# Performance work log

Hardware: AMD Instinct MI355X
Metric: run time of the kernel (lower is better)

The kernel has to match this reference:

```python
import jax, jax.numpy as jnp
import numpy as np

CHUNK = 64  # mamba chunk size


def _ssd_chunk_scan(x, dt, A, Bs, Cs, R):
    """Exact chunked selective scan (mamba_chunk_scan_combined math, no D skip).
    x: [B,L,H,P] (H=K*R heads), dt: [B,L,H] (already softplus'd),
    A: [H], Bs/Cs: [B,L,K,N] groups (head h uses group h//R).
    Returns y: [B,L,H,P]."""
    Bsz, L, Hh, P = x.shape
    K, N = Bs.shape[2], Bs.shape[3]
    Nc = L // CHUNK
    # broadcast groups -> heads (head k*R+r uses group k)
    Bh = jnp.repeat(Bs, R, axis=2)  # [B,L,H,N]
    Ch = jnp.repeat(Cs, R, axis=2)
    xc = x.reshape(Bsz, Nc, CHUNK, Hh, P)
    dtc = dt.reshape(Bsz, Nc, CHUNK, Hh)
    Bc = Bh.reshape(Bsz, Nc, CHUNK, Hh, N)
    Cc = Ch.reshape(Bsz, Nc, CHUNK, Hh, N)
    dA = jnp.transpose(dtc, (0, 1, 3, 2)) * A[None, None, :, None]  # [B,Nc,H,Q]
    Acum = jnp.cumsum(dA, axis=-1)
    # intra-chunk decay matrix Lmat[i,j] = exp(sum_{j<s<=i} dA_s), lower-tri
    diff = Acum[..., :, None] - Acum[..., None, :]  # [B,Nc,H,Q,Q]
    tri = jnp.tril(jnp.ones((CHUNK, CHUNK), bool))
    Lmat = jnp.where(tri, jnp.exp(diff), 0.0)
    xdt = xc * dtc[..., None]  # dt enters as dt_j * B_j * x_j
    Y_diag = jnp.einsum('bcqhn,bcshn,bchqs,bcshp->bcqhp', Cc, Bc, Lmat, xdt)
    # chunk end states
    decay_last = jnp.exp(Acum[..., -1:] - Acum)  # [B,Nc,H,Q]
    states = jnp.einsum('bcqhn,bchq,bcqhp->bchpn', Bc, decay_last, xdt)
    chunk_decay = jnp.exp(Acum[..., -1])  # [B,Nc,H]
    def step(S, inp):
        cd, st = inp
        return cd[..., None, None] * S + st, S  # emit state BEFORE this chunk
    S0 = jnp.zeros((Bsz, Hh, P, N), x.dtype)
    _, prev = jax.lax.scan(step, S0, (jnp.moveaxis(chunk_decay, 1, 0), jnp.moveaxis(states, 1, 0)))
    prev = jnp.moveaxis(prev, 0, 1)  # [B,Nc,H,P,N]
    Y_off = jnp.einsum('bcqhn,bchpn,bchq->bcqhp', Cc, prev, jnp.exp(Acum))
    return (Y_diag + Y_off).reshape(Bsz, L, Hh, P)


def _forward(x, in_proj_w, conv_w, conv_b, x_proj_w, A_logs, Ds, dt_bias,
             out_norm_g, out_norm_b, out_proj_w):
    B, H, W, Dm = x.shape
    K, R = A_logs.shape
    P = Ds.shape[2]               # headdim
    d_inner = x_proj_w.shape[2]
    N = (x_proj_w.shape[1] - R) // 2
    L = H * W
    # in_proj + gate split
    xz = jnp.einsum('bhwc,dc->bhwd', x, in_proj_w)
    xi, z = jnp.split(xz, 2, axis=-1)
    z = jax.nn.gelu(z, approximate=False)
    # depthwise 3x3 conv (torch weight [d_inner,1,3,3] -> HWIO [3,3,1,d_inner])
    kern = jnp.transpose(conv_w, (2, 3, 1, 0))
    xi = jax.lax.conv_general_dilated(xi, kern, (1, 1), 'SAME',
            dimension_numbers=('NHWC', 'HWIO', 'NHWC'),
            feature_group_count=d_inner) + conv_b
    xi = jax.nn.gelu(xi, approximate=False)
    # cross2d scan: row-major, col-major, and their reverses
    x0 = xi.reshape(B, L, d_inner)
    x1 = jnp.transpose(xi, (0, 2, 1, 3)).reshape(B, L, d_inner)
    xs = jnp.stack([x0, x1, x0[:, ::-1], x1[:, ::-1]], axis=2)  # [B,L,K,d_inner]
    x_dbl = jnp.einsum('blkd,kcd->blkc', xs, x_proj_w)
    dts = x_dbl[..., :R].reshape(B, L, K * R)
    Bs = x_dbl[..., R:R + N]
    Cs = x_dbl[..., R + N:]
    xs_h = xs.reshape(B, L, K * R, P)
    A = -jnp.exp(A_logs.astype(jnp.float32)).reshape(K * R)
    Dmat = Ds.astype(jnp.float32).reshape(K * R, P)
    dt = jax.nn.softplus(dts + dt_bias.reshape(K * R))
    ys = _ssd_chunk_scan(xs_h, dt, A, Bs, Cs, R) + xs_h * Dmat  # D skip on raw x
    ys = ys.reshape(B, L, K, d_inner)
    # cross merge: invert each scan order, sum over K
    def unT(y):
        return jnp.transpose(y.reshape(B, W, H, d_inner), (0, 2, 1, 3)).reshape(B, L, d_inner)
    y = ys[:, :, 0] + ys[:, ::-1, 2] + unT(ys[:, :, 1]) + unT(ys[:, ::-1, 3])
    # out LayerNorm
    y = y.reshape(B, H, W, d_inner)
    mu = y.mean(-1, keepdims=True)
    var = y.var(-1, keepdims=True)
    y = (y - mu) / jnp.sqrt(var + 1e-5) * out_norm_g + out_norm_b
    y = y * z  # gating
    return jnp.einsum('bhwd,cd->bhwc', y, out_proj_w)


def setup_inputs() -> dict:
    key = jax.random.key(0)
    ks = jax.random.split(key, 10)
    B, H, W, Dm = 2, 64, 64, 192
    d_inner, K, R, N = 384, 4, 12, 64
    P = d_inner // R  # 32
    s = 0.02
    return {
        'x': jax.random.normal(ks[0], (B, H, W, Dm), jnp.float32),
        'in_proj_w': s * jax.random.normal(ks[1], (2 * d_inner, Dm), jnp.float32),
        'conv_w': s * jax.random.normal(ks[2], (d_inner, 1, 3, 3), jnp.float32),
        'conv_b': s * jax.random.normal(ks[3], (d_inner,), jnp.float32),
        'x_proj_w': s * jax.random.normal(ks[4], (K, R + 2 * N, d_inner), jnp.float32),
        'A_logs': 0.5 * jax.random.normal(ks[5], (K, R), jnp.float32),
        'Ds': jax.random.uniform(ks[6], (K, R, P), jnp.float32),
        'dt_bias': 0.1 * jax.random.uniform(ks[7], (K, R), jnp.float32),
        'out_norm_g': jnp.ones((d_inner,), jnp.float32),
        'out_norm_b': jnp.zeros((d_inner,), jnp.float32),
        'out_proj_w': s * jax.random.normal(ks[8], (Dm, d_inner), jnp.float32),
    }


def reference(x, in_proj_w, conv_w, conv_b, x_proj_w, A_logs, Ds, dt_bias,
              out_norm_g, out_norm_b, out_proj_w):
    return _forward(x, in_proj_w, conv_w, conv_b, x_proj_w, A_logs, Ds, dt_bias,
                    out_norm_g, out_norm_b, out_proj_w)
```

## Files before the change

### kernel.cpp

```cpp
#include <hip/hip_runtime.h>
#include <math.h>

#define DI 384

typedef __attribute__((ext_vector_type(8))) short bf8v;
typedef __attribute__((ext_vector_type(4))) float f4v;

__device__ __forceinline__ f4v mfma16(bf8v a, bf8v b, f4v c) {
  return __builtin_amdgcn_mfma_f32_16x16x32_bf16(a, b, c, 0, 0, 0);
}

__device__ __forceinline__ int trf(int l) { return ((l & 63) << 6) | (l >> 6); }
__device__ __forceinline__ int mapk(int k, int l) {
  if (k == 0) return l;
  if (k == 1) return trf(l);
  if (k == 2) return 4095 - l;
  return trf(4095 - l);
}
__device__ __forceinline__ float gelu_f(float x) {
  return 0.5f * x * (1.0f + erff(x * 0.7071067811865475f));
}
__device__ __forceinline__ float softplus_f(float x) {
  return (x > 20.0f) ? x : log1pf(expf(x));
}
__device__ __forceinline__ unsigned short f2bf(float f) {
  unsigned u = __float_as_uint(f);
  unsigned r = (u + 0x7fff + ((u >> 16) & 1)) >> 16;
  return (unsigned short)r;
}
__device__ __forceinline__ float bf2f(unsigned short h) {
  return __uint_as_float(((unsigned)h) << 16);
}
__device__ __forceinline__ int swz(int row, int col) {
  return (row << 6) + ((((col >> 3) ^ (row & 7)) << 3) | (col & 7));
}
__device__ __forceinline__ int foff(int row, int cb) {
  return (row << 6) + ((cb ^ (row & 7)) << 3);
}

__global__ __launch_bounds__(256) void k_cvt(const float* __restrict__ src,
                                             unsigned short* __restrict__ hi,
                                             unsigned short* __restrict__ lo, int n) {
  int i = blockIdx.x * 256 + threadIdx.x;
  if (i >= n) return;
  float v = src[i];
  unsigned short h = f2bf(v);
  hi[i] = h;
  lo[i] = f2bf(v - bf2f(h));
}

__global__ __launch_bounds__(256) void k_inproj(const unsigned short* __restrict__ Ahi,
                                                const unsigned short* __restrict__ Alo,
                                                const unsigned short* __restrict__ Whi,
                                                const unsigned short* __restrict__ Wlo,
                                                float* __restrict__ xi_raw,
                                                float* __restrict__ zg) {
  const int K = 192;
  __shared__ unsigned short Ah[4096], Al[4096], Bh[4096], Bl[4096];
  int tid = threadIdx.x;
  int lane = tid & 63, w = tid >> 6;
  int cl = lane & 15, kb = lane >> 4;
  int wm = w >> 1, wn = w & 1;
  int m0 = blockIdx.y * 64, n0 = blockIdx.x * 64;
  f4v acc[2][2];
  acc[0][0] = acc[0][1] = acc[1][0] = acc[1][1] = (f4v){0.f, 0.f, 0.f, 0.f};
  for (int k0 = 0; k0 < K; k0 += 64) {
#pragma unroll
    for (int u = 0; u < 2; ++u) {
      int unit = tid + u * 256;
      int row = unit >> 3, blk = unit & 7;
      int e = foff(row, blk);
      size_t ga = (size_t)(m0 + row) * K + k0 + blk * 8;
      size_t gb = (size_t)(n0 + row) * K + k0 + blk * 8;
      *(bf8v*)(Ah + e) = *(const bf8v*)(Ahi + ga);
      *(bf8v*)(Al + e) = *(const bf8v*)(Alo + ga);
      *(bf8v*)(Bh + e) = *(const bf8v*)(Whi + gb);
      *(bf8v*)(Bl + e) = *(const bf8v*)(Wlo + gb);
    }
    __syncthreads();
#pragma unroll
    for (int chunk = 0; chunk < 2; ++chunk) {
      int cb = chunk * 4 + kb;
      bf8v ah[2], al[2], bh[2], bl[2];
#pragma unroll
      for (int mi = 0; mi < 2; ++mi) {
        ah[mi] = *(const bf8v*)(Ah + foff(wm * 32 + mi * 16 + cl, cb));
        al[mi] = *(const bf8v*)(Al + foff(wm * 32 + mi * 16 + cl, cb));
      }
#pragma unroll
      for (int ni = 0; ni < 2; ++ni) {
        bh[ni] = *(const bf8v*)(Bh + foff(wn * 32 + ni * 16 + cl, cb));
        bl[ni] = *(const bf8v*)(Bl + foff(wn * 32 + ni * 16 + cl, cb));
      }
#pragma unroll
      for (int mi = 0; mi < 2; ++mi)
#pragma unroll
        for (int ni = 0; ni < 2; ++ni) {
          acc[mi][ni] = mfma16(ah[mi], bh[ni], acc[mi][ni]);
          acc[mi][ni] = mfma16(ah[mi], bl[ni], acc[mi][ni]);
          acc[mi][ni] = mfma16(al[mi], bh[ni], acc[mi][ni]);
        }
    }
    __syncthreads();
  }
#pragma unroll
  for (int mi = 0; mi < 2; ++mi)
#pragma unroll
    for (int ni = 0; ni < 2; ++ni)
#pragma unroll
      for (int i = 0; i < 4; ++i) {
        int m = m0 + wm * 32 + mi * 16 + kb * 4 + i;
        int n = n0 + wn * 32 + ni * 16 + cl;
        float v = acc[mi][ni][i];
        if (n < DI) xi_raw[(size_t)m * DI + n] = v;
        else zg[(size_t)m * DI + (n - DI)] = gelu_f(v);
      }
}

__global__ __launch_bounds__(256) void k_conv(const float* __restrict__ xin,
                                              const float* __restrict__ cw,
                                              const float* __restrict__ cb,
                                              unsigned short* __restrict__ xhi,
                                              unsigned short* __restrict__ xlo) {
  int idx = blockIdx.x * 256 + threadIdx.x;
  int c = idx % DI;
  int lf = idx / DI;
  int b = lf >> 12;
  int l = lf & 4095;
  int h = l >> 6, w = l & 63;
  float acc = cb[c];
#pragma unroll
  for (int dh = -1; dh <= 1; ++dh) {
    int hh = h + dh;
    if ((unsigned)hh >= 64u) continue;
#pragma unroll
    for (int dw = -1; dw <= 1; ++dw) {
      int ww = w + dw;
      if ((unsigned)ww >= 64u) continue;
      acc += xin[((size_t)((b << 12) | (hh << 6) | ww)) * DI + c] *
             cw[c * 9 + (dh + 1) * 3 + (dw + 1)];
    }
  }
  float g = gelu_f(acc);
  unsigned short hv = f2bf(g);
  xhi[(size_t)idx] = hv;
  xlo[(size_t)idx] = f2bf(g - bf2f(hv));
}

__global__ __launch_bounds__(256) void k_xproj(const unsigned short* __restrict__ xhi,
                                               const unsigned short* __restrict__ xlo,
                                               const unsigned short* __restrict__ Whi,
                                               const unsigned short* __restrict__ Wlo,
                                               const float* __restrict__ dt_bias,
                                               float* __restrict__ dt_buf,
                                               unsigned short* __restrict__ Bhi,
                                               unsigned short* __restrict__ Blo,
                                               unsigned short* __restrict__ Chi,
                                               unsigned short* __restrict__ Clo) {
  const int K = DI, N = 140;
  int kdir = blockIdx.z;
  __shared__ unsigned short Ah[4096], Al[4096], Bh[4096], Bl[4096];
  __shared__ int rowbase[64];
  int tid = threadIdx.x;
  int lane = tid & 63, w = tid >> 6;
  int cl = lane & 15, kb = lane >> 4;
  int wm = w >> 1, wn = w & 1;
  int m0 = blockIdx.y * 64, n0 = blockIdx.x * 64;
  if (tid < 64) {
    int m = m0 + tid;
    int b = m >> 12, l = m & 4095;
    rowbase[tid] = (b << 12) + mapk(kdir, l);
  }
  const unsigned short* wkh = Whi + (size_t)kdir * N * K;
  const unsigned short* wkl = Wlo + (size_t)kdir * N * K;
  f4v acc[2][2];
  acc[0][0] = acc[0][1] = acc[1][0] = acc[1][1] = (f4v){0.f, 0.f, 0.f, 0.f};
  __syncthreads();
  for (int k0 = 0; k0 < K; k0 += 64) {
#pragma unroll
    for (int u = 0; u < 2; ++u) {
      int unit = tid + u * 256;
      int row = unit >> 3, blk = unit & 7;
      int e = foff(row, blk);
      size_t ga = (size_t)rowbase[row] * K + k0 + blk * 8;
      *(bf8v*)(Ah + e) = *(const bf8v*)(xhi + ga);
      *(bf8v*)(Al + e) = *(const bf8v*)(xlo + ga);
      int n = n0 + row;
      if (n < N) {
        size_t gb = (size_t)n * K + k0 + blk * 8;
        *(bf8v*)(Bh + e) = *(const bf8v*)(wkh + gb);
        *(bf8v*)(Bl + e) = *(const bf8v*)(wkl + gb);
      } else {
        bf8v z = {0, 0, 0, 0, 0, 0, 0, 0};
        *(bf8v*)(Bh + e) = z;
        *(bf8v*)(Bl + e) = z;
      }
    }
    __syncthreads();
#pragma unroll
    for (int chunk = 0; chunk < 2; ++chunk) {
      int cb = chunk * 4 + kb;
      bf8v ah[2], al[2], bh[2], bl[2];
#pragma unroll
      for (int mi = 0; mi < 2; ++mi) {
        ah[mi] = *(const bf8v*)(Ah + foff(wm * 32 + mi * 16 + cl, cb));
        al[mi] = *(const bf8v*)(Al + foff(wm * 32 + mi * 16 + cl, cb));
      }
#pragma unroll
      for (int ni = 0; ni < 2; ++ni) {
        bh[ni] = *(const bf8v*)(Bh + foff(wn * 32 + ni * 16 + cl, cb));
        bl[ni] = *(const bf8v*)(Bl + foff(wn * 32 + ni * 16 + cl, cb));
      }
#pragma unroll
      for (int mi = 0; mi < 2; ++mi)
#pragma unroll
        for (int ni = 0; ni < 2; ++ni) {
          acc[mi][ni] = mfma16(ah[mi], bh[ni], acc[mi][ni]);
          acc[mi][ni] = mfma16(ah[mi], bl[ni], acc[mi][ni]);
          acc[mi][ni] = mfma16(al[mi], bh[ni], acc[mi][ni]);
        }
    }
    __syncthreads();
  }
#pragma unroll
  for (int mi = 0; mi < 2; ++mi)
#pragma unroll
    for (int ni = 0; ni < 2; ++ni)
#pragma unroll
      for (int i = 0; i < 4; ++i) {
        int m = m0 + wm * 32 + mi * 16 + kb * 4 + i;
        int n = n0 + wn * 32 + ni * 16 + cl;
        if (n >= N) continue;
        float v = acc[mi][ni][i];
        int b = m >> 12, l = m & 4095;
        if (n < 12) {
          dt_buf[(((size_t)(b * 48 + kdir * 12 + n)) << 12) + l] =
              softplus_f(v + dt_bias[kdir * 12 + n]);
        } else if (n < 76) {
          size_t off = (((size_t)((b * 4 + kdir) << 12)) + l) * 64 + (n - 12);
          unsigned short hh = f2bf(v);
          Bhi[off] = hh;
          Blo[off] = f2bf(v - bf2f(hh));
        } else {
          size_t off = (((size_t)((b * 4 + kdir) << 12)) + l) * 64 + (n - 76);
          unsigned short hh = f2bf(v);
          Chi[off] = hh;
          Clo[off] = f2bf(v - bf2f(hh));
        }
      }
}

__global__ __launch_bounds__(256) void k_states(const unsigned short* __restrict__ xhi,
                                                const unsigned short* __restrict__ xlo,
                                                const float* __restrict__ dt_buf,
                                                const unsigned short* __restrict__ Bhi,
                                                const unsigned short* __restrict__ Blo,
                                                const float* __restrict__ A_logs,
                                                unsigned short* __restrict__ Shi,
                                                float* __restrict__ cdec) {
  int c = blockIdx.x, k = blockIdx.y >> 1, g = blockIdx.y & 1, b = blockIdx.z;
  __shared__ unsigned short Bt_h[4096], Bt_l[4096];
  __shared__ unsigned short xw_h[2048], xw_l[2048];
  int tid = threadIdx.x;
  int lane = tid & 63, w = tid >> 6;
  int cl = lane & 15, kb = lane >> 4;
  size_t Bbase = (((size_t)((b * 4 + k) << 12)) + c * 64) * 64;
  {
    int n = lane;
#pragma unroll
    for (int it = 0; it < 8; ++it) {
      int q0 = 2 * (w + it * 4);
      unsigned short h0 = Bhi[Bbase + (size_t)q0 * 64 + n];
      unsigned short h1 = Bhi[Bbase + (size_t)(q0 + 1) * 64 + n];
      unsigned short l0 = Blo[Bbase + (size_t)q0 * 64 + n];
      unsigned short l1 = Blo[Bbase + (size_t)(q0 + 1) * 64 + n];
      int e = swz(n, q0);
      *(unsigned int*)(Bt_h + e) = (unsigned)h0 | ((unsigned)h1 << 16);
      *(unsigned int*)(Bt_l + e) = (unsigned)l0 | ((unsigned)l1 << 16);
    }
  }
  int p_s = tid & 31, qg = tid >> 5;
  for (int rr = 0; rr < 6; ++rr) {
    int r = g * 6 + rr;
    int h = k * 12 + r;
    unsigned short rh0[4], rh1[4], rl0[4], rl1[4];
#pragma unroll
    for (int it = 0; it < 4; ++it) {
      int q0 = 2 * (qg + it * 8);
      int l0 = mapk(k, c * 64 + q0), l1 = mapk(k, c * 64 + q0 + 1);
      size_t o0 = ((size_t)((b << 12) + l0)) * DI + r * 32 + p_s;
      size_t o1 = ((size_t)((b << 12) + l1)) * DI + r * 32 + p_s;
      rh0[it] = xhi[o0];
      rl0[it] = xlo[o0];
      rh1[it] = xhi[o1];
      rl1[it] = xlo[o1];
    }
    float dtv = dt_buf[(((size_t)(b * 48 + h)) << 12) + c * 64 + lane];
    float v = dtv * (-__expf(A_logs[h]));
#pragma unroll
    for (int off = 1; off < 64; off <<= 1) {
      float u = __shfl_up(v, off, 64);
      if (lane >= off) v += u;
    }
    float alast = __shfl(v, 63, 64);
    float wq = dtv * __expf(alast - v);
    if (tid == 63) cdec[(b * 48 + h) * 64 + c] = __expf(alast);
    __syncthreads();
#pragma unroll
    for (int it = 0; it < 4; ++it) {
      int q0 = 2 * (qg + it * 8);
      float w0 = __shfl(wq, q0, 64), w1 = __shfl(wq, q0 + 1, 64);
      float x0 = (bf2f(rh0[it]) + bf2f(rl0[it])) * w0;
      float x1 = (bf2f(rh1[it]) + bf2f(rl1[it])) * w1;
      unsigned short h0 = f2bf(x0), h1 = f2bf(x1);
      unsigned short L0 = f2bf(x0 - bf2f(h0)), L1 = f2bf(x1 - bf2f(h1));
      int e = swz(p_s, q0);
      *(unsigned int*)(xw_h + e) = (unsigned)h0 | ((unsigned)h1 << 16);
      *(unsigned int*)(xw_l + e) = (unsigned)L0 | ((unsigned)L1 << 16);
    }
    __syncthreads();
    f4v acc0 = {0.f, 0.f, 0.f, 0.f}, acc1 = {0.f, 0.f, 0.f, 0.f};
#pragma unroll
    for (int chunk = 0; chunk < 2; ++chunk) {
      int cb_ = chunk * 4 + kb;
      int nrow = w * 16 + cl;
      bf8v bh = *(const bf8v*)(Bt_h + foff(nrow, cb_));
      bf8v bl = *(const bf8v*)(Bt_l + foff(nrow, cb_));
      bf8v a0h = *(const bf8v*)(xw_h + foff(cl, cb_));
      bf8v a0l = *(const bf8v*)(xw_l + foff(cl, cb_));
      bf8v a1h = *(const bf8v*)(xw_h + foff(16 + cl, cb_));
      bf8v a1l = *(const bf8v*)(xw_l + foff(16 + cl, cb_));
      acc0 = mfma16(a0h, bh, acc0);
      acc0 = mfma16(a0h, bl, acc0);
      acc0 = mfma16(a0l, bh, acc0);
      acc1 = mfma16(a1h, bh, acc1);
      acc1 = mfma16(a1h, bl, acc1);
      acc1 = mfma16(a1l, bh, acc1);
    }
    size_t sbase = ((size_t)(b * 48 + h) * 64 + c) * 2048;
#pragma unroll
    for (int i = 0; i < 4; ++i) {
      int prow = kb * 4 + i;
      int n = w * 16 + cl;
      Shi[sbase + (size_t)prow * 64 + n] = f2bf(acc0[i]);
      Shi[sbase + (size_t)(16 + prow) * 64 + n] = f2bf(acc1[i]);
    }
  }
}

__global__ __launch_bounds__(256) void k_scan(unsigned short* __restrict__ Shi,
                                              const float* __restrict__ cdec) {
  int j = blockIdx.x;
  int bh = blockIdx.y;
  int tid = threadIdx.x;
  size_t base0 = (size_t)bh * 64 * 2048 + j * 256 + tid;
  float S = 0.0f;
  float nxt = bf2f(Shi[base0]);
  for (int c = 0; c < 64; ++c) {
    float cd = cdec[bh * 64 + c];
    size_t idx = base0 + (size_t)c * 2048;
    float tmp = nxt;
    if (c < 63) nxt = bf2f(Shi[idx + 2048]);
    Shi[idx] = f2bf(S);
    S = cd * S + tmp;
  }
}

__global__ __launch_bounds__(256) void k_out(const unsigned short* __restrict__ xhi,
                                             const unsigned short* __restrict__ xlo,
                                             const float* __restrict__ dt_buf,
                                             const unsigned short* __restrict__ Bhi,
                                             const unsigned short* __restrict__ Blo,
                                             const unsigned short* __restrict__ Chi,
                                             const unsigned short* __restrict__ Clo,
                                             const float* __restrict__ A_logs,
                                             const float* __restrict__ Ds,
                                             const unsigned short* __restrict__ Phi,
                                             float* __restrict__ ys) {
  int c = blockIdx.x, k = blockIdx.y >> 1, g = blockIdx.y & 1, b = blockIdx.z;
  __shared__ unsigned short C_h[4096], C_l[4096];
  __shared__ unsigned short G_h[4096];
  __shared__ unsigned short Xbuf[4096];
  unsigned short* X_h = Xbuf;
  unsigned short* X_l = Xbuf + 2048;
  int tid = threadIdx.x;
  int lane = tid & 63, w = tid >> 6;
  int cl = lane & 15, kb = lane >> 4;
  size_t base64 = (((size_t)((b * 4 + k) << 12)) + c * 64) * 64;
  {
    int n0 = (tid & 31) * 2;
    int qq = tid >> 5;
#pragma unroll
    for (int it = 0; it < 8; ++it) {
      int q = qq + it * 8;
      size_t off = base64 + (size_t)q * 64 + n0;
      int e = swz(q, n0);
      *(unsigned int*)(C_h + e) = *(const unsigned int*)(Chi + off);
      *(unsigned int*)(C_l + e) = *(const unsigned int*)(Clo + off);
      *(unsigned int*)(G_h + e) = *(const unsigned int*)(Bhi + off);
      *(unsigned int*)(Xbuf + e) = *(const unsigned int*)(Blo + off);
    }
  }
  __syncthreads();
  bf8v caf_h[2], caf_l[2];
#pragma unroll
  for (int chunk = 0; chunk < 2; ++chunk) {
    caf_h[chunk] = *(const bf8v*)(C_h + foff(w * 16 + cl, chunk * 4 + kb));
    caf_l[chunk] = *(const bf8v*)(C_l + foff(w * 16 + cl, chunk * 4 + kb));
  }
  f4v cbt[4];
#pragma unroll
  for (int St = 0; St < 4; ++St) cbt[St] = (f4v){0.f, 0.f, 0.f, 0.f};
#pragma unroll
  for (int St = 0; St < 4; ++St) {
    int srow = St * 16 + cl;
#pragma unroll
    for (int chunk = 0; chunk < 2; ++chunk) {
      bf8v bh = *(const bf8v*)(G_h + foff(srow, chunk * 4 + kb));
      bf8v bl = *(const bf8v*)(Xbuf + foff(srow, chunk * 4 + kb));
      cbt[St] = mfma16(caf_h[chunk], bh, cbt[St]);
      cbt[St] = mfma16(caf_h[chunk], bl, cbt[St]);
      cbt[St] = mfma16(caf_l[chunk], bh, cbt[St]);
    }
  }
  int p_s = tid & 31, sg = tid >> 5;
  int h0_ = k * 12 + g * 6;
  bf8v pfA[2][2], pfB[2][2];
  {
    size_t pb = ((size_t)(b * 48 + h0_) * 64 + c) * 2048;
#pragma unroll
    for (int chunk = 0; chunk < 2; ++chunk) {
      int cb_ = chunk * 4 + kb;
      pfA[chunk][0] = *(const bf8v*)(Phi + pb + (size_t)cl * 64 + cb_ * 8);
      pfA[chunk][1] = *(const bf8v*)(Phi + pb + (size_t)(16 + cl) * 64 + cb_ * 8);
    }
  }
  float dtA = dt_buf[(((size_t)(b * 48 + h0_)) << 12) + c * 64 + lane];
  float dtB;
  for (int rr = 0; rr < 6; ++rr) {
    int r = g * 6 + rr;
    int h = k * 12 + r;
    float dtv = dtA;
    float v = dtv * (-__expf(A_logs[h]));
#pragma unroll
    for (int off = 1; off < 64; off <<= 1) {
      float u = __shfl_up(v, off, 64);
      if (lane >= off) v += u;
    }
    float ea = __expf(v);
    __syncthreads();
#pragma unroll
    for (int it = 0; it < 4; ++it) {
      int s0 = 2 * (sg + it * 8);
      int l0 = mapk(k, c * 64 + s0), l1 = mapk(k, c * 64 + s0 + 1);
      size_t o0 = ((size_t)((b << 12) + l0)) * DI + r * 32 + p_s;
      size_t o1 = ((size_t)((b << 12) + l1)) * DI + r * 32 + p_s;
      int e = swz(p_s, s0);
      *(unsigned int*)(X_h + e) = (unsigned)xhi[o0] | ((unsigned)xhi[o1] << 16);
      *(unsigned int*)(X_l + e) = (unsigned)xlo[o0] | ((unsigned)xlo[o1] << 16);
    }
    float vq[4];
#pragma unroll
    for (int i = 0; i < 4; ++i) vq[i] = __shfl(v, w * 16 + kb * 4 + i, 64);
#pragma unroll
    for (int St = 0; St < 4; ++St) {
      int s = St * 16 + cl;
      float vs = __shfl(v, s, 64);
      float dts = __shfl(dtv, s, 64);
#pragma unroll
      for (int i = 0; i < 4; ++i) {
        int q = w * 16 + kb * 4 + i;
        float gv = (q >= s) ? cbt[St][i] * __expf(vq[i] - vs) * dts : 0.0f;
        G_h[swz(q, s)] = f2bf(gv);
      }
    }
    __syncthreads();
    if (rr < 5) {
      size_t pbn = ((size_t)(b * 48 + h + 1) * 64 + c) * 2048;
#pragma unroll
      for (int chunk = 0; chunk < 2; ++chunk) {
        int cb_ = chunk * 4 + kb;
        pfB[chunk][0] = *(const bf8v*)(Phi + pbn + (size_t)cl * 64 + cb_ * 8);
        pfB[chunk][1] = *(const bf8v*)(Phi + pbn + (size_t)(16 + cl) * 64 + cb_ * 8);
      }
      dtB = dt_buf[(((size_t)(b * 48 + h + 1)) << 12) + c * 64 + lane];
    }
    f4v aD0 = {0.f, 0.f, 0.f, 0.f}, aD1 = aD0, aO0 = aD0, aO1 = aD0;
#pragma unroll
    for (int chunk = 0; chunk < 2; ++chunk) {
      int cb_ = chunk * 4 + kb;
      int qrow = w * 16 + cl;
      bf8v gh = *(const bf8v*)(G_h + foff(qrow, cb_));
      bf8v x0h = *(const bf8v*)(X_h + foff(cl, cb_));
      bf8v x0l = *(const bf8v*)(X_l + foff(cl, cb_));
      bf8v x1h = *(const bf8v*)(X_h + foff(16 + cl, cb_));
      bf8v x1l = *(const bf8v*)(X_l + foff(16 + cl, cb_));
      aD0 = mfma16(gh, x0h, aD0);
      aD0 = mfma16(gh, x0l, aD0);
      aD1 = mfma16(gh, x1h, aD1);
      aD1 = mfma16(gh, x1l, aD1);
      aO0 = mfma16(caf_h[chunk], pfA[chunk][0], aO0);
      aO0 = mfma16(caf_l[chunk], pfA[chunk][0], aO0);
      aO1 = mfma16(caf_h[chunk], pfA[chunk][1], aO1);
      aO1 = mfma16(caf_l[chunk], pfA[chunk][1], aO1);
    }
    float D0 = Ds[h * 32 + cl], D1 = Ds[h * 32 + 16 + cl];
    size_t ybase = ((size_t)((b * 4 + k) << 12) + c * 64) * DI + r * 32;
#pragma unroll
    for (int i = 0; i < 4; ++i) {
      int q = w * 16 + kb * 4 + i;
      float eaq = __shfl(ea, q, 64);
      int e0 = swz(cl, q), e1 = swz(16 + cl, q);
      float xv0 = bf2f(X_h[e0]) + bf2f(X_l[e0]);
      float xv1 = bf2f(X_h[e1]) + bf2f(X_l[e1]);
      ys[ybase + (size_t)q * DI + cl] = aD0[i] + eaq * aO0[i] + D0 * xv0;
      ys[ybase + (size_t)q * DI + 16 + cl] = aD1[i] + eaq * aO1[i] + D1 * xv1;
    }
#pragma unroll
    for (int chunk = 0; chunk < 2; ++chunk) {
      pfA[chunk][0] = pfB[chunk][0];
      pfA[chunk][1] = pfB[chunk][1];
    }
    dtA = dtB;
  }
}

__global__ __launch_bounds__(128) void k_ln(const float* __restrict__ ys,
                                            const float* __restrict__ zg,
                                            const float* __restrict__ gg,
                                            const float* __restrict__ bb,
                                            unsigned short* __restrict__ y2h,
                                            unsigned short* __restrict__ y2l) {
  int row = blockIdx.x;
  int b = row >> 12, l = row & 4095;
  int l1 = trf(l);
  int l2 = 4095 - l;
  int l3 = 4095 - l1;
  int tid = threadIdx.x;
  float v[3];
  size_t base = ((size_t)(b * 4)) << 12;
#pragma unroll
  for (int j = 0; j < 3; ++j) {
    int d = tid + j * 128;
    v[j] = ys[(base + l) * DI + d] + ys[(base + 4096 + l1) * DI + d] +
           ys[(base + 8192 + l2) * DI + d] + ys[(base + 12288 + l3) * DI + d];
  }
  __shared__ float red[2];
  float s = v[0] + v[1] + v[2];
#pragma unroll
  for (int off = 32; off > 0; off >>= 1) s += __shfl_down(s, off, 64);
  if ((tid & 63) == 0) red[tid >> 6] = s;
  __syncthreads();
  float mu = (red[0] + red[1]) * (1.0f / 384.0f);
  __syncthreads();
  float d2 = 0.0f;
#pragma unroll
  for (int j = 0; j < 3; ++j) {
    float dd = v[j] - mu;
    d2 += dd * dd;
  }
#pragma unroll
  for (int off = 32; off > 0; off >>= 1) d2 += __shfl_down(d2, off, 64);
  if ((tid & 63) == 0) red[tid >> 6] = d2;
  __syncthreads();
  float rstd = rsqrtf((red[0] + red[1]) * (1.0f / 384.0f) + 1e-5f);
#pragma unroll
  for (int j = 0; j < 3; ++j) {
    int d = tid + j * 128;
    float yv = (v[j] - mu) * rstd * gg[d] + bb[d];
    float o = yv * zg[(size_t)row * DI + d];
    unsigned short hh = f2bf(o);
    y2h[(size_t)row * DI + d] = hh;
    y2l[(size_t)row * DI + d] = f2bf(o - bf2f(hh));
  }
}

__global__ __launch_bounds__(256) void k_outproj(const unsigned short* __restrict__ Ahi,
                                                 const unsigned short* __restrict__ Alo,
                                                 const unsigned short* __restrict__ Whi,
                                                 const unsigned short* __restrict__ Wlo,
                                                 float* __restrict__ out) {
  const int K = DI, NO = 192;
  __shared__ unsigned short Ah[4096], Al[4096], Bh[4096], Bl[4096];
  int tid = threadIdx.x;
  int lane = tid & 63, w = tid >> 6;
  int cl = lane & 15, kb = lane >> 4;
  int wm = w >> 1, wn = w & 1;
  int m0 = blockIdx.y * 64, n0 = blockIdx.x * 64;
  f4v acc[2][2];
  acc[0][0] = acc[0][1] = acc[1][0] = acc[1][1] = (f4v){0.f, 0.f, 0.f, 0.f};
  for (int k0 = 0; k0 < K; k0 += 64) {
#pragma unroll
    for (int u = 0; u < 2; ++u) {
      int unit = tid + u * 256;
      int row = unit >> 3, blk = unit & 7;
      int e = foff(row, blk);
      size_t ga = (size_t)(m0 + row) * K + k0 + blk * 8;
      size_t gb = (size_t)(n0 + row) * K + k0 + blk * 8;
      *(bf8v*)(Ah + e) = *(const bf8v*)(Ahi + ga);
      *(bf8v*)(Al + e) = *(const bf8v*)(Alo + ga);
      *(bf8v*)(Bh + e) = *(const bf8v*)(Whi + gb);
      *(bf8v*)(Bl + e) = *(const bf8v*)(Wlo + gb);
    }
    __syncthreads();
#pragma unroll
    for (int chunk = 0; chunk < 2; ++chunk) {
      int cb = chunk * 4 + kb;
      bf8v ah[2], al[2], bh[2], bl[2];
#pragma unroll
      for (int mi = 0; mi < 2; ++mi) {
        ah[mi] = *(const bf8v*)(Ah + foff(wm * 32 + mi * 16 + cl, cb));
        al[mi] = *(const bf8v*)(Al + foff(wm * 32 + mi * 16 + cl, cb));
      }
#pragma unroll
      for (int ni = 0; ni < 2; ++ni) {
        bh[ni] = *(const bf8v*)(Bh + foff(wn * 32 + ni * 16 + cl, cb));
        bl[ni] = *(const bf8v*)(Bl + foff(wn * 32 + ni * 16 + cl, cb));
      }
#pragma unroll
      for (int mi = 0; mi < 2; ++mi)
#pragma unroll
        for (int ni = 0; ni < 2; ++ni) {
          acc[mi][ni] = mfma16(ah[mi], bh[ni], acc[mi][ni]);
          acc[mi][ni] = mfma16(ah[mi], bl[ni], acc[mi][ni]);
          acc[mi][ni] = mfma16(al[mi], bh[ni], acc[mi][ni]);
        }
    }
    __syncthreads();
  }
#pragma unroll
  for (int mi = 0; mi < 2; ++mi)
#pragma unroll
    for (int ni = 0; ni < 2; ++ni)
#pragma unroll
      for (int i = 0; i < 4; ++i) {
        int m = m0 + wm * 32 + mi * 16 + kb * 4 + i;
        int n = n0 + wn * 32 + ni * 16 + cl;
        out[(size_t)m * NO + n] = acc[mi][ni][i];
      }
}

extern "C" void kernel_launch(void* const* d_in, const int* in_sizes, int n_in,
                              void* d_out, int out_size, void* d_ws, size_t ws_size,
                              hipStream_t stream) {
  const float* x = (const float*)d_in[0];
  const float* in_proj_w = (const float*)d_in[1];
  const float* conv_w = (const float*)d_in[2];
  const float* conv_b = (const float*)d_in[3];
  const float* x_proj_w = (const float*)d_in[4];
  const float* A_logs = (const float*)d_in[5];
  const float* Ds = (const float*)d_in[6];
  const float* dt_bias = (const float*)d_in[7];
  const float* out_norm_g = (const float*)d_in[8];
  const float* out_norm_b = (const float*)d_in[9];
  const float* out_proj_w = (const float*)d_in[10];
  float* out = (float*)d_out;

  float* ws = (float*)d_ws;
  float* xi_raw = ws;
  float* zg = xi_raw + 3145728;
  float* dt_buf = zg + 3145728;
  float* cdec = dt_buf + 393216;
  float* ys = cdec + 6144;
  unsigned short* u16p = (unsigned short*)(ys + 12582912);
  unsigned short* Shi = u16p;    u16p += 12582912;
  unsigned short* xi_hi = u16p;  u16p += 3145728;
  unsigned short* xi_lo = u16p;  u16p += 3145728;
  unsigned short* x_hi = u16p;   u16p += 1572864;
  unsigned short* x_lo = u16p;   u16p += 1572864;
  unsigned short* win_hi = u16p; u16p += 147456;
  unsigned short* win_lo = u16p; u16p += 147456;
  unsigned short* wxp_hi = u16p; u16p += 215040;
  unsigned short* wxp_lo = u16p; u16p += 215040;
  unsigned short* wout_hi = u16p; u16p += 73728;
  unsigned short* wout_lo = u16p; u16p += 73728;
  unsigned short* Bhi = u16p;    u16p += 2097152;
  unsigned short* Blo = u16p;    u16p += 2097152;
  unsigned short* Chi = u16p;    u16p += 2097152;
  unsigned short* Clo = u16p;    u16p += 2097152;
  unsigned short* y2h = (unsigned short*)xi_raw;
  unsigned short* y2l = y2h + 3145728;

  k_cvt<<<(1572864 + 255) / 256, 256, 0, stream>>>(x, x_hi, x_lo, 1572864);
  k_cvt<<<(147456 + 255) / 256, 256, 0, stream>>>(in_proj_w, win_hi, win_lo, 147456);
  k_cvt<<<(215040 + 255) / 256, 256, 0, stream>>>(x_proj_w, wxp_hi, wxp_lo, 215040);
  k_cvt<<<(73728 + 255) / 256, 256, 0, stream>>>(out_proj_w, wout_hi, wout_lo, 73728);

  k_inproj<<<dim3(12, 128), 256, 0, stream>>>(x_hi, x_lo, win_hi, win_lo, xi_raw, zg);
  k_conv<<<dim3(12288), 256, 0, stream>>>(xi_raw, conv_w, conv_b, xi_hi, xi_lo);
  k_xproj<<<dim3(3, 128, 4), 256, 0, stream>>>(xi_hi, xi_lo, wxp_hi, wxp_lo, dt_bias,
                                               dt_buf, Bhi, Blo, Chi, Clo);
  k_states<<<dim3(64, 8, 2), 256, 0, stream>>>(xi_hi, xi_lo, dt_buf, Bhi, Blo, A_logs,
                                               Shi, cdec);
  k_scan<<<dim3(8, 96), 256, 0, stream>>>(Shi, cdec);
  k_out<<<dim3(64, 8, 2), 256, 0, stream>>>(xi_hi, xi_lo, dt_buf, Bhi, Blo, Chi, Clo,
                                            A_logs, Ds, Shi, ys);
  k_ln<<<dim3(8192), 128, 0, stream>>>(ys, zg, out_norm_g, out_norm_b, y2h, y2l);
  k_outproj<<<dim3(3, 128), 256, 0, stream>>>(y2h, y2l, wout_hi, wout_lo, out);
}
```

Measured before the change: 201.4 us.

## Add transposed x copy, precompute dt cumsum, drop low-bf16 terms in states

```diff
diff --git a/kernel.cpp b/kernel.cpp
--- a/kernel.cpp
+++ b/kernel.cpp
@@ -121,7 +121,9 @@
                                               const float* __restrict__ cw,
                                               const float* __restrict__ cb,
                                               unsigned short* __restrict__ xhi,
-                                              unsigned short* __restrict__ xlo) {
+                                              unsigned short* __restrict__ xlo,
+                                              unsigned short* __restrict__ xthi,
+                                              unsigned short* __restrict__ xtlo) {
   int idx = blockIdx.x * 256 + threadIdx.x;
   int c = idx % DI;
   int lf = idx / DI;
@@ -143,8 +145,12 @@
   }
   float g = gelu_f(acc);
   unsigned short hv = f2bf(g);
+  unsigned short lv = f2bf(g - bf2f(hv));
   xhi[(size_t)idx] = hv;
-  xlo[(size_t)idx] = f2bf(g - bf2f(hv));
+  xlo[(size_t)idx] = lv;
+  size_t tof = ((size_t)((b << 12) | trf(l))) * DI + c;
+  xthi[tof] = hv;
+  xtlo[tof] = lv;
 }
 
 __global__ __launch_bounds__(256) void k_xproj(const unsigned short* __restrict__ xhi,
@@ -250,17 +256,35 @@
       }
 }
 
+__global__ __launch_bounds__(256) void k_dtacum(const float* __restrict__ dt_buf,
+                                                const float* __restrict__ A_logs,
+                                                float* __restrict__ ac_buf,
+                                                float* __restrict__ cdec) {
+  int bh = blockIdx.y;
+  int c = blockIdx.x * 4 + (threadIdx.x >> 6);
+  int lane = threadIdx.x & 63;
+  int h = bh % 48;
+  size_t o = ((size_t)bh << 12) + c * 64 + lane;
+  float dtv = dt_buf[o];
+  float v = dtv * (-__expf(A_logs[h]));
+#pragma unroll
+  for (int off = 1; off < 64; off <<= 1) {
+    float u = __shfl_up(v, off, 64);
+    if (lane >= off) v += u;
+  }
+  ac_buf[o] = v;
+  if (lane == 63) cdec[bh * 64 + c] = __expf(v);
+}
+
 __global__ __launch_bounds__(256) void k_states(const unsigned short* __restrict__ xhi,
-                                                const unsigned short* __restrict__ xlo,
+                                                const unsigned short* __restrict__ xthi,
                                                 const float* __restrict__ dt_buf,
+                                                const float* __restrict__ ac_buf,
                                                 const unsigned short* __restrict__ Bhi,
-                                                const unsigned short* __restrict__ Blo,
-                                                const float* __restrict__ A_logs,
-                                                unsigned short* __restrict__ Shi,
-                                                float* __restrict__ cdec) {
+                                                unsigned short* __restrict__ Shi) {
   int c = blockIdx.x, k = blockIdx.y >> 1, g = blockIdx.y & 1, b = blockIdx.z;
-  __shared__ unsigned short Bt_h[4096], Bt_l[4096];
-  __shared__ unsigned short xw_h[2048], xw_l[2048];
+  __shared__ unsigned short Bt_h[4096];
+  __shared__ unsigned short xw_h[2048];
   int tid = threadIdx.x;
   int lane = tid & 63, w = tid >> 6;
   int cl = lane & 15, kb = lane >> 4;
@@ -272,70 +296,47 @@
       int q0 = 2 * (w + it * 4);
       unsigned short h0 = Bhi[Bbase + (size_t)q0 * 64 + n];
       unsigned short h1 = Bhi[Bbase + (size_t)(q0 + 1) * 64 + n];
-      unsigned short l0 = Blo[Bbase + (size_t)q0 * 64 + n];
-      unsigned short l1 = Blo[Bbase + (size_t)(q0 + 1) * 64 + n];
-      int e = swz(n, q0);
-      *(unsigned int*)(Bt_h + e) = (unsigned)h0 | ((unsigned)h1 << 16);
-      *(unsigned int*)(Bt_l + e) = (unsigned)l0 | ((unsigned)l1 << 16);
-    }
-  }
+      *(unsigned int*)(Bt_h + swz(n, q0)) = (unsigned)h0 | ((unsigned)h1 << 16);
+    }
+  }
+  const unsigned short* xp = (k & 1) ? xthi : xhi;
   int p_s = tid & 31, qg = tid >> 5;
   for (int rr = 0; rr < 6; ++rr) {
     int r = g * 6 + rr;
     int h = k * 12 + r;
-    unsigned short rh0[4], rh1[4], rl0[4], rl1[4];
+    unsigned short rh0[4], rh1[4];
 #pragma unroll
     for (int it = 0; it < 4; ++it) {
       int q0 = 2 * (qg + it * 8);
-      int l0 = mapk(k, c * 64 + q0), l1 = mapk(k, c * 64 + q0 + 1);
-      size_t o0 = ((size_t)((b << 12) + l0)) * DI + r * 32 + p_s;
-      size_t o1 = ((size_t)((b << 12) + l1)) * DI + r * 32 + p_s;
-      rh0[it] = xhi[o0];
-      rl0[it] = xlo[o0];
-      rh1[it] = xhi[o1];
-      rl1[it] = xlo[o1];
-    }
-    float dtv = dt_buf[(((size_t)(b * 48 + h)) << 12) + c * 64 + lane];
-    float v = dtv * (-__expf(A_logs[h]));
-#pragma unroll
-    for (int off = 1; off < 64; off <<= 1) {
-      float u = __shfl_up(v, off, 64);
-      if (lane >= off) v += u;
-    }
+      int i0 = c * 64 + q0, i1 = i0 + 1;
+      if (k & 2) { i0 = 4095 - i0; i1 = 4094 - (i1 - 1) - 1 + 0; i1 = 4095 - (c * 64 + q0 + 1); }
+      rh0[it] = xp[((size_t)((b << 12) + i0)) * DI + r * 32 + p_s];
+      rh1[it] = xp[((size_t)((b << 12) + i1)) * DI + r * 32 + p_s];
+    }
+    size_t dto = (((size_t)(b * 48 + h)) << 12) + c * 64 + lane;
+    float dtv = dt_buf[dto];
+    float v = ac_buf[dto];
     float alast = __shfl(v, 63, 64);
     float wq = dtv * __expf(alast - v);
-    if (tid == 63) cdec[(b * 48 + h) * 64 + c] = __expf(alast);
     __syncthreads();
 #pragma unroll
     for (int it = 0; it < 4; ++it) {
       int q0 = 2 * (qg + it * 8);
       float w0 = __shfl(wq, q0, 64), w1 = __shfl(wq, q0 + 1, 64);
-      float x0 = (bf2f(rh0[it]) + bf2f(rl0[it])) * w0;
-      float x1 = (bf2f(rh1[it]) + bf2f(rl1[it])) * w1;
-      unsigned short h0 = f2bf(x0), h1 = f2bf(x1);
-      unsigned short L0 = f2bf(x0 - bf2f(h0)), L1 = f2bf(x1 - bf2f(h1));
-      int e = swz(p_s, q0);
-      *(unsigned int*)(xw_h + e) = (unsigned)h0 | ((unsigned)h1 << 16);
-      *(unsigned int*)(xw_l + e) = (unsigned)L0 | ((unsigned)L1 << 16);
+      unsigned short h0 = f2bf(bf2f(rh0[it]) * w0);
+      unsigned short h1 = f2bf(bf2f(rh1[it]) * w1);
+      *(unsigned int*)(xw_h + swz(p_s, q0)) = (unsigned)h0 | ((unsigned)h1 << 16);
     }
     __syncthreads();
     f4v acc0 = {0.f, 0.f, 0.f, 0.f}, acc1 = {0.f, 0.f, 0.f, 0.f};
 #pragma unroll
     for (int chunk = 0; chunk < 2; ++chunk) {
       int cb_ = chunk * 4 + kb;
-      int nrow = w * 16 + cl;
-      bf8v bh = *(const bf8v*)(Bt_h + foff(nrow, cb_));
-      bf8v bl = *(const bf8v*)(Bt_l + foff(nrow, cb_));
+      bf8v bh = *(const bf8v*)(Bt_h + foff(w * 16 + cl, cb_));
       bf8v a0h = *(const bf8v*)(xw_h + foff(cl, cb_));
-      bf8v a0l = *(const bf8v*)(xw_l + foff(cl, cb_));
       bf8v a1h = *(const bf8v*)(xw_h + foff(16 + cl, cb_));
-      bf8v a1l = *(const bf8v*)(xw_l + foff(16 + cl, cb_));
       acc0 = mfma16(a0h, bh, acc0);
-      acc0 = mfma16(a0h, bl, acc0);
-      acc0 = mfma16(a0l, bh, acc0);
       acc1 = mfma16(a1h, bh, acc1);
-      acc1 = mfma16(a1h, bl, acc1);
-      acc1 = mfma16(a1l, bh, acc1);
     }
     size_t sbase = ((size_t)(b * 48 + h) * 64 + c) * 2048;
 #pragma unroll
@@ -368,12 +369,14 @@
 
 __global__ __launch_bounds__(256) void k_out(const unsigned short* __restrict__ xhi,
                                              const unsigned short* __restrict__ xlo,
+                                             const unsigned short* __restrict__ xthi,
+                                             const unsigned short* __restrict__ xtlo,
                                              const float* __restrict__ dt_buf,
+                                             const float* __restrict__ ac_buf,
                                              const unsigned short* __restrict__ Bhi,
                                              const unsigned short* __restrict__ Blo,
                                              const unsigned short* __restrict__ Chi,
                                              const unsigned short* __restrict__ Clo,
-                                             const float* __restrict__ A_logs,
                                              const float* __restrict__ Ds,
                                              const unsigned short* __restrict__ Phi,
                                              float* __restrict__ ys) {
@@ -423,6 +426,8 @@
       cbt[St] = mfma16(caf_l[chunk], bh, cbt[St]);
     }
   }
+  const unsigned short* xph = (k & 1) ? xthi : xhi;
+  const unsigned short* xpl = (k & 1) ? xtlo : xlo;
   int p_s = tid & 31, sg = tid >> 5;
   int h0_ = k * 12 + g * 6;
   bf8v pfA[2][2], pfB[2][2];
@@ -435,29 +440,27 @@
       pfA[chunk][1] = *(const bf8v*)(Phi + pb + (size_t)(16 + cl) * 64 + cb_ * 8);
     }
   }
-  float dtA = dt_buf[(((size_t)(b * 48 + h0_)) << 12) + c * 64 + lane];
-  float dtB;
+  size_t dto0 = (((size_t)(b * 48 + h0_)) << 12) + c * 64 + lane;
+  float dtA = dt_buf[dto0];
+  float vA = ac_buf[dto0];
+  float dtB, vB;
   for (int rr = 0; rr < 6; ++rr) {
     int r = g * 6 + rr;
     int h = k * 12 + r;
     float dtv = dtA;
-    float v = dtv * (-__expf(A_logs[h]));
-#pragma unroll
-    for (int off = 1; off < 64; off <<= 1) {
-      float u = __shfl_up(v, off, 64);
-      if (lane >= off) v += u;
-    }
+    float v = vA;
     float ea = __expf(v);
     __syncthreads();
 #pragma unroll
     for (int it = 0; it < 4; ++it) {
       int s0 = 2 * (sg + it * 8);
-      int l0 = mapk(k, c * 64 + s0), l1 = mapk(k, c * 64 + s0 + 1);
-      size_t o0 = ((size_t)((b << 12) + l0)) * DI + r * 32 + p_s;
-      size_t o1 = ((size_t)((b << 12) + l1)) * DI + r * 32 + p_s;
+      int i0 = c * 64 + s0, i1 = i0 + 1;
+      if (k & 2) { i0 = 4095 - i0; i1 = i0 - 1; }
+      size_t o0 = ((size_t)((b << 12) + i0)) * DI + r * 32 + p_s;
+      size_t o1 = ((size_t)((b << 12) + i1)) * DI + r * 32 + p_s;
       int e = swz(p_s, s0);
-      *(unsigned int*)(X_h + e) = (unsigned)xhi[o0] | ((unsigned)xhi[o1] << 16);
-      *(unsigned int*)(X_l + e) = (unsigned)xlo[o0] | ((unsigned)xlo[o1] << 16);
+      *(unsigned int*)(X_h + e) = (unsigned)xph[o0] | ((unsigned)xph[o1] << 16);
+      *(unsigned int*)(X_l + e) = (unsigned)xpl[o0] | ((unsigned)xpl[o1] << 16);
     }
     float vq[4];
 #pragma unroll
@@ -483,7 +486,9 @@
         pfB[chunk][0] = *(const bf8v*)(Phi + pbn + (size_t)cl * 64 + cb_ * 8);
         pfB[chunk][1] = *(const bf8v*)(Phi + pbn + (size_t)(16 + cl) * 64 + cb_ * 8);
       }
-      dtB = dt_buf[(((size_t)(b * 48 + h + 1)) << 12) + c * 64 + lane];
+      size_t dton = (((size_t)(b * 48 + h + 1)) << 12) + c * 64 + lane;
+      dtB = dt_buf[dton];
+      vB = ac_buf[dton];
     }
     f4v aD0 = {0.f, 0.f, 0.f, 0.f}, aD1 = aD0, aO0 = aD0, aO1 = aD0;
 #pragma unroll
@@ -522,6 +527,7 @@
       pfA[chunk][1] = pfB[chunk][1];
     }
     dtA = dtB;
+    vA = vB;
   }
 }
 
@@ -660,7 +666,8 @@
   float* xi_raw = ws;
   float* zg = xi_raw + 3145728;
   float* dt_buf = zg + 3145728;
-  float* cdec = dt_buf + 393216;
+  float* ac_buf = dt_buf + 393216;
+  float* cdec = ac_buf + 393216;
   float* ys = cdec + 6144;
   unsigned short* u16p = (unsigned short*)(ys + 12582912);
   unsigned short* Shi = u16p;    u16p += 12582912;
@@ -668,6 +675,7 @@
   unsigned short* xi_lo = u16p;  u16p += 3145728;
   unsigned short* x_hi = u16p;   u16p += 1572864;
   unsigned short* x_lo = u16p;   u16p += 1572864;
+  unsigned short* xit_lo = u16p; u16p += 3145728;
   unsigned short* win_hi = u16p; u16p += 147456;
   unsigned short* win_lo = u16p; u16p += 147456;
   unsigned short* wxp_hi = u16p; u16p += 215040;
@@ -678,6 +686,7 @@
   unsigned short* Blo = u16p;    u16p += 2097152;
   unsigned short* Chi = u16p;    u16p += 2097152;
   unsigned short* Clo = u16p;    u16p += 2097152;
+  unsigned short* xit_hi = x_hi;
   unsigned short* y2h = (unsigned short*)xi_raw;
   unsigned short* y2l = y2h + 3145728;
 
@@ -687,14 +696,15 @@
   k_cvt<<<(73728 + 255) / 256, 256, 0, stream>>>(out_proj_w, wout_hi, wout_lo, 73728);
 
   k_inproj<<<dim3(12, 128), 256, 0, stream>>>(x_hi, x_lo, win_hi, win_lo, xi_raw, zg);
-  k_conv<<<dim3(12288), 256, 0, stream>>>(xi_raw, conv_w, conv_b, xi_hi, xi_lo);
+  k_conv<<<dim3(12288), 256, 0, stream>>>(xi_raw, conv_w, conv_b, xi_hi, xi_lo,
+                                          xit_hi, xit_lo);
   k_xproj<<<dim3(3, 128, 4), 256, 0, stream>>>(xi_hi, xi_lo, wxp_hi, wxp_lo, dt_bias,
                                                dt_buf, Bhi, Blo, Chi, Clo);
-  k_states<<<dim3(64, 8, 2), 256, 0, stream>>>(xi_hi, xi_lo, dt_buf, Bhi, Blo, A_logs,
-                                               Shi, cdec);
+  k_dtacum<<<dim3(16, 96), 256, 0, stream>>>(dt_buf, A_logs, ac_buf, cdec);
+  k_states<<<dim3(64, 8, 2), 256, 0, stream>>>(xi_hi, xit_hi, dt_buf, ac_buf, Bhi, Shi);
   k_scan<<<dim3(8, 96), 256, 0, stream>>>(Shi, cdec);
-  k_out<<<dim3(64, 8, 2), 256, 0, stream>>>(xi_hi, xi_lo, dt_buf, Bhi, Blo, Chi, Clo,
-                                            A_logs, Ds, Shi, ys);
+  k_out<<<dim3(64, 8, 2), 256, 0, stream>>>(xi_hi, xi_lo, xit_hi, xit_lo, dt_buf,
+                                            ac_buf, Bhi, Blo, Chi, Clo, Ds, Shi, ys);
   k_ln<<<dim3(8192), 128, 0, stream>>>(ys, zg, out_norm_g, out_norm_b, y2h, y2l);
   k_outproj<<<dim3(3, 128), 256, 0, stream>>>(y2h, y2l, wout_hi, wout_lo, out);
 }
```

Result: no change. 198.1 us (-1.6%).
